# Kernel tuning notes

Hardware: AMD Instinct MI355X
Metric: run time of the kernel (lower is better)

The kernel has to match this reference:

```python
import jax, jax.numpy as jnp
import numpy as np

N = 50000        # nodes
E = 1600000      # edges
R = 20           # relations (num_rels, num_bases == num_rels -> per-relation weights)
IN = 4           # in_dim
H = 64           # hidden_dim
L = 4            # total RGCN layers (num_hidden_layers=3 hidden + 1 output)
EPS = 1e-5       # BatchNorm eps


def setup_inputs() -> dict:
    key = jax.random.key(0)
    ks = jax.random.split(key, 14)
    x = jax.random.normal(ks[0], (N, IN), jnp.float32)
    edge_index = jax.random.randint(ks[1], (2, E), 0, N, jnp.int32)
    edge_type = jax.random.randint(ks[2], (E,), 0, R, jnp.int32)
    # RGCN layer 0: in_dim -> hidden
    W0 = jax.random.normal(ks[3], (R, IN, H), jnp.float32) * 0.1
    root0 = jax.random.normal(ks[4], (IN, H), jnp.float32) * 0.1
    b0 = jax.random.normal(ks[5], (H,), jnp.float32) * 0.1
    # RGCN layers 1..3: hidden -> hidden (stacked)
    Wh = jax.random.normal(ks[6], (L - 1, R, H, H), jnp.float32) * 0.1
    rooth = jax.random.normal(ks[7], (L - 1, H, H), jnp.float32) * 0.1
    bh = jax.random.normal(ks[8], (L - 1, H), jnp.float32) * 0.1
    # BatchNorm (eval mode: running stats) per layer
    gamma = 1.0 + 0.1 * jax.random.normal(ks[9], (L, H), jnp.float32)
    beta = 0.1 * jax.random.normal(ks[10], (L, H), jnp.float32)
    run_mean = 0.1 * jax.random.normal(ks[11], (L, H), jnp.float32)
    run_var = jax.random.uniform(ks[12], (L, H), jnp.float32, 0.5, 1.5)
    return {"x": x, "edge_index": edge_index, "edge_type": edge_type,
            "W0": W0, "root0": root0, "b0": b0,
            "Wh": Wh, "rooth": rooth, "bh": bh,
            "gamma": gamma, "beta": beta,
            "run_mean": run_mean, "run_var": run_var}


def _rgcn(h, src, dst, seg, inv_cnt, W, root, bias):
    # mean-aggregate source features per (relation, dst) segment, then per-relation GEMM
    msum = jax.ops.segment_sum(h[src], seg, num_segments=R * N)  # [R*N, F]
    agg = (msum * inv_cnt).reshape(R, N, -1)                     # [R, N, F]
    return jnp.einsum('rni,rio->no', agg, W) + h @ root + bias   # [N, out]


def _bn_eval(h, g, b, rm, rv):
    return (h - rm) * (g * jax.lax.rsqrt(rv + EPS)) + b


def reference(x, edge_index, edge_type, W0, root0, b0, Wh, rooth, bh,
              gamma, beta, run_mean, run_var):
    src, dst = edge_index[0], edge_index[1]
    seg = edge_type * N + dst  # [E], segment id per (relation, dst)
    cnt = jax.ops.segment_sum(jnp.ones((E,), x.dtype), seg, num_segments=R * N)
    inv_cnt = (1.0 / jnp.maximum(cnt, 1.0))[:, None]  # mean aggregation per relation
    h = x
    for i in range(L):
        W, root, b = (W0, root0, b0) if i == 0 else (Wh[i - 1], rooth[i - 1], bh[i - 1])
        h = _rgcn(h, src, dst, seg, inv_cnt, W, root, b)
        h = _bn_eval(h, gamma[i], beta[i], run_mean[i], run_var[i])
    # last layer (i == num_hidden_layers): relu (dropout is identity in eval)
    return jax.nn.relu(h)
```

## Files before the change

### kernel.cpp

```cpp
#include <hip/hip_runtime.h>

#define NN 50000
#define NE 1600000
#define RR 20
#define BN_EPS 1e-5f
#define SCAN_NB ((NN + 1023) / 1024)

typedef __attribute__((ext_vector_type(8))) short bf16x8;
typedef __attribute__((ext_vector_type(4))) float f32x4;

__device__ __forceinline__ unsigned short f2bf(float f) {
    unsigned u = __float_as_uint(f);
    u += 0x7fff + ((u >> 16) & 1);
    return (unsigned short)(u >> 16);
}
__device__ __forceinline__ void unpack8(uint4 r, float* v) {
    v[0] = __uint_as_float(r.x << 16); v[1] = __uint_as_float(r.x & 0xffff0000u);
    v[2] = __uint_as_float(r.y << 16); v[3] = __uint_as_float(r.y & 0xffff0000u);
    v[4] = __uint_as_float(r.z << 16); v[5] = __uint_as_float(r.z & 0xffff0000u);
    v[6] = __uint_as_float(r.w << 16); v[7] = __uint_as_float(r.w & 0xffff0000u);
}

__global__ void count_kernel(const int* __restrict__ dst, const int* __restrict__ et,
                             int* __restrict__ cnt) {
    int stride = gridDim.x * blockDim.x;
    for (int e = blockIdx.x * blockDim.x + threadIdx.x; e < NE; e += stride)
        atomicAdd(&cnt[dst[e] * RR + et[e]], 1);
}

__global__ void deg_kernel(const int* __restrict__ cnt, int* __restrict__ deg) {
    int stride = gridDim.x * blockDim.x;
    for (int n = blockIdx.x * blockDim.x + threadIdx.x; n < NN; n += stride) {
        int s = 0;
        #pragma unroll
        for (int r = 0; r < RR; ++r) s += cnt[n * RR + r];
        deg[n] = s;
    }
}

__global__ __launch_bounds__(256) void scan1_kernel(const int* __restrict__ in,
                                                    int* __restrict__ out,
                                                    int* __restrict__ bsums, int n) {
    __shared__ int lds[256];
    int tid  = threadIdx.x;
    int base = blockIdx.x * 1024 + tid * 4;
    int v[4];
    #pragma unroll
    for (int j = 0; j < 4; ++j) v[j] = (base + j < n) ? in[base + j] : 0;
    int tsum = v[0] + v[1] + v[2] + v[3];
    lds[tid] = tsum;
    __syncthreads();
    for (int off = 1; off < 256; off <<= 1) {
        int t = (tid >= off) ? lds[tid - off] : 0;
        __syncthreads();
        lds[tid] += t;
        __syncthreads();
    }
    int run = lds[tid] - tsum;
    #pragma unroll
    for (int j = 0; j < 4; ++j) {
        if (base + j < n) out[base + j] = run;
        run += v[j];
    }
    if (tid == 255) bsums[blockIdx.x] = lds[255];
}

__global__ __launch_bounds__(1024) void scan_top_kernel(int* __restrict__ bsums, int nb) {
    __shared__ int lds[1024];
    int tid = threadIdx.x;
    int v = (tid < nb) ? bsums[tid] : 0;
    lds[tid] = v;
    __syncthreads();
    for (int off = 1; off < 1024; off <<= 1) {
        int t = (tid >= off) ? lds[tid - off] : 0;
        __syncthreads();
        lds[tid] += t;
        __syncthreads();
    }
    bsums[tid] = lds[tid] - v;
}

__global__ void scan_add_kernel(int* __restrict__ out, const int* __restrict__ bsums, int n) {
    int stride = gridDim.x * blockDim.x;
    int i = blockIdx.x * blockDim.x + threadIdx.x;
    if (i == 0) out[NN] = NE;
    for (; i < n; i += stride)
        out[i] += bsums[i >> 10];
}

__global__ void fill_kernel(const int* __restrict__ src, const int* __restrict__ dst,
                            const int* __restrict__ et, const int* __restrict__ offs,
                            const int* __restrict__ cntdr,
                            int* __restrict__ fill, uint2* __restrict__ ep) {
    int stride = gridDim.x * blockDim.x;
    for (int e = blockIdx.x * blockDim.x + threadIdx.x; e < NE; e += stride) {
        int d = dst[e], r = et[e];
        int pos = offs[d] + atomicAdd(&fill[d], 1);
        int c = cntdr[d * RR + r];
        float ic = 1.0f / (float)(c > 0 ? c : 1);
        ep[pos] = make_uint2((unsigned)src[e] | ((unsigned)r << 20),
                             __float_as_uint(ic));
    }
}

__global__ __launch_bounds__(256) void wprep_kernel(const float* __restrict__ Wh,
                                                    const float* __restrict__ rooth,
                                                    unsigned short* __restrict__ Wt) {
    int l = blockIdx.x / 21, r = blockIdx.x % 21;
    const float* Ws = (r < 20) ? Wh + ((size_t)l * 20 + r) * 4096
                               : rooth + (size_t)l * 4096;
    unsigned short* Wd = Wt + ((size_t)l * 21 + r) * 4096;
    int t = threadIdx.x;
    int n4 = (t & 15) * 4;
    for (int k = t >> 4; k < 64; k += 16) {
        float4 w = *(const float4*)&Ws[(size_t)k * 64 + n4];
        Wd[(n4 + 0) * 64 + k] = f2bf(w.x);
        Wd[(n4 + 1) * 64 + k] = f2bf(w.y);
        Wd[(n4 + 2) * 64 + k] = f2bf(w.z);
        Wd[(n4 + 3) * 64 + k] = f2bf(w.w);
    }
}

__global__ __launch_bounds__(256) void xform0_kernel(
    const float* __restrict__ x, const float* __restrict__ W0,
    const float* __restrict__ root0, unsigned short* __restrict__ T,
    int c0, int nr) {
    __shared__ float Wl[21 * 256];
    int tid = threadIdx.x;
    for (int i = tid; i < 21 * 256; i += 256)
        Wl[i] = (i < 20 * 256) ? W0[i] : root0[i - 20 * 256];
    __syncthreads();
    int wslot = (blockIdx.x * 256 + tid) >> 6;
    int nw    = (gridDim.x * 256) >> 6;
    int col   = tid & 63;
    for (int n = wslot; n < NN; n += nw) {
        float4 xv = *(const float4*)&x[(size_t)n * 4];
        for (int r = 0; r < nr; ++r) {
            const float* w = &Wl[(c0 + r) * 256];
            float acc = xv.x * w[col] + xv.y * w[64 + col] +
                        xv.z * w[128 + col] + xv.w * w[192 + col];
            T[((size_t)r * NN + n) * 64 + col] = f2bf(acc);
        }
    }
}

__global__ __launch_bounds__(256) void xform_kernel(
    const unsigned short* __restrict__ hin, const unsigned short* __restrict__ WtL,
    unsigned short* __restrict__ T, int c0, int nr) {
    __shared__ unsigned short tile[64 * 72];
    const int tid  = threadIdx.x;
    const int n0   = blockIdx.x * 64;
    const int wv   = tid >> 6;
    const int lane = tid & 63;
    const int frow = lane & 15;
    const int kgrp = lane >> 4;
    int arc = min(n0 + wv * 16 + frow, NN - 1);
    bf16x8 a0 = *(const bf16x8*)&hin[(size_t)arc * 64 + kgrp * 8];
    bf16x8 a1 = *(const bf16x8*)&hin[(size_t)arc * 64 + 32 + kgrp * 8];
    for (int r = 0; r < nr; ++r) {
        const unsigned short* Wr = WtL + (size_t)(c0 + r) * 4096;
        unsigned short* Tr = T + (size_t)r * NN * 64;
        #pragma unroll
        for (int cf = 0; cf < 4; ++cf) {
            bf16x8 b0 = *(const bf16x8*)&Wr[(cf * 16 + frow) * 64 + kgrp * 8];
            bf16x8 b1 = *(const bf16x8*)&Wr[(cf * 16 + frow) * 64 + 32 + kgrp * 8];
            f32x4 d = {0.f, 0.f, 0.f, 0.f};
            d = __builtin_amdgcn_mfma_f32_16x16x32_bf16(a0, b0, d, 0, 0, 0);
            d = __builtin_amdgcn_mfma_f32_16x16x32_bf16(a1, b1, d, 0, 0, 0);
            #pragma unroll
            for (int j = 0; j < 4; ++j)
                tile[(wv * 16 + kgrp * 4 + j) * 72 + cf * 16 + frow] = f2bf(d[j]);
        }
        __syncthreads();
        #pragma unroll
        for (int i = tid; i < 512; i += 256) {
            int row = i >> 3, c16 = i & 7;
            int node = n0 + row;
            if (node < NN)
                *(uint4*)&Tr[(size_t)node * 64 + c16 * 8] =
                    *(const uint4*)&tile[row * 72 + c16 * 8];
        }
        __syncthreads();
    }
}

template <bool FIRST, bool LASTP, bool LASTL>
__global__ __launch_bounds__(256) void agg_kernel(
    const unsigned short* __restrict__ T, const int* __restrict__ offs,
    const uint2* __restrict__ ep, float* __restrict__ accum, int c0, int c1,
    const float* __restrict__ bias, const float* __restrict__ gamma,
    const float* __restrict__ beta, const float* __restrict__ rmean,
    const float* __restrict__ rvar, unsigned short* __restrict__ outb,
    float* __restrict__ outf) {
    constexpr bool FULL = FIRST && LASTP;
    int wid   = (blockIdx.x * 256 + threadIdx.x) >> 6;
    int nw    = (gridDim.x * 256) >> 6;
    int lane  = threadIdx.x & 63;
    int eslot = lane >> 3;
    int flane = lane & 7;
    const unsigned ce = (c1 < RR) ? (unsigned)c1 : (unsigned)RR;

    for (int n = wid; n < NN; n += nw) {
        int e0 = offs[n], e1 = offs[n + 1];
        float a[8] = {0, 0, 0, 0, 0, 0, 0, 0};
        for (int e = e0 + eslot; e < e1; e += 8) {
            uint2 m = ep[e];
            unsigned r = m.x >> 20;
            if (FULL || (r >= (unsigned)c0 && r < ce)) {
                float ic = __uint_as_float(m.y);
                size_t ti = ((size_t)(r - c0) * NN + (m.x & 0xFFFFF)) * 64;
                uint4 row = *(const uint4*)&T[ti + flane * 8];
                float v[8]; unpack8(row, v);
                #pragma unroll
                for (int j = 0; j < 8; ++j) a[j] += ic * v[j];
            }
        }
        #pragma unroll
        for (int off = 8; off < 64; off <<= 1)
            #pragma unroll
            for (int j = 0; j < 8; ++j) a[j] += __shfl_xor(a[j], off);

        if (eslot == 0) {
            if (LASTP) {
                uint4 rr = *(const uint4*)&T[((size_t)(20 - c0) * NN + n) * 64 + flane * 8];
                float rv[8]; unpack8(rr, rv);
                #pragma unroll
                for (int j = 0; j < 8; ++j) a[j] += rv[j];
            }
            if (!FIRST) {
                float4 p0 = *(const float4*)&accum[(size_t)n * 64 + flane * 8];
                float4 p1 = *(const float4*)&accum[(size_t)n * 64 + flane * 8 + 4];
                a[0] += p0.x; a[1] += p0.y; a[2] += p0.z; a[3] += p0.w;
                a[4] += p1.x; a[5] += p1.y; a[6] += p1.z; a[7] += p1.w;
            }
            if (!LASTP) {
                *(float4*)&accum[(size_t)n * 64 + flane * 8] =
                    make_float4(a[0], a[1], a[2], a[3]);
                *(float4*)&accum[(size_t)n * 64 + flane * 8 + 4] =
                    make_float4(a[4], a[5], a[6], a[7]);
            } else {
                float v[8];
                #pragma unroll
                for (int j = 0; j < 8; ++j) {
                    int col = flane * 8 + j;
                    float s = gamma[col] * rsqrtf(rvar[col] + BN_EPS);
                    v[j] = (a[j] + bias[col] - rmean[col]) * s + beta[col];
                }
                if (LASTL) {
                    float4 o0 = make_float4(fmaxf(v[0],0.f), fmaxf(v[1],0.f),
                                            fmaxf(v[2],0.f), fmaxf(v[3],0.f));
                    float4 o1 = make_float4(fmaxf(v[4],0.f), fmaxf(v[5],0.f),
                                            fmaxf(v[6],0.f), fmaxf(v[7],0.f));
                    *(float4*)&outf[(size_t)n * 64 + flane * 8]     = o0;
                    *(float4*)&outf[(size_t)n * 64 + flane * 8 + 4] = o1;
                } else {
                    ushort4 p0, p1;
                    p0.x = f2bf(v[0]); p0.y = f2bf(v[1]);
                    p0.z = f2bf(v[2]); p0.w = f2bf(v[3]);
                    p1.x = f2bf(v[4]); p1.y = f2bf(v[5]);
                    p1.z = f2bf(v[6]); p1.w = f2bf(v[7]);
                    *(ushort4*)&outb[(size_t)n * 64 + flane * 8]     = p0;
                    *(ushort4*)&outb[(size_t)n * 64 + flane * 8 + 4] = p1;
                }
            }
        }
    }
}

extern "C" void kernel_launch(void* const* d_in, const int* in_sizes, int n_in,
                              void* d_out, int out_size, void* d_ws, size_t ws_size,
                              hipStream_t stream) {
    const float* x     = (const float*)d_in[0];
    const int*   ei    = (const int*)d_in[1];
    const int*   et    = (const int*)d_in[2];
    const float* W0    = (const float*)d_in[3];
    const float* root0 = (const float*)d_in[4];
    const float* b0    = (const float*)d_in[5];
    const float* Wh    = (const float*)d_in[6];
    const float* rooth = (const float*)d_in[7];
    const float* bh    = (const float*)d_in[8];
    const float* gamma = (const float*)d_in[9];
    const float* beta  = (const float*)d_in[10];
    const float* rmean = (const float*)d_in[11];
    const float* rvar  = (const float*)d_in[12];
    float* out = (float*)d_out;

    const int* src = ei;
    const int* dst = ei + NE;

    int*   cntdr = (int*)d_ws;
    int*   deg   = cntdr + 1000000;
    int*   fill  = deg + 50000;
    int*   offs  = fill + 50000;
    int*   bsums = offs + 50004;
    uint2* ep    = (uint2*)(bsums + 1024);
    unsigned short* Wt = (unsigned short*)(ep + NE);
    unsigned short* h0 = Wt + 3 * 21 * 4096;
    unsigned short* h1 = h0 + NN * 64;
    float* accum = (float*)(h1 + NN * 64);
    unsigned short* T = (unsigned short*)(accum + NN * 64);

    size_t used  = (size_t)((char*)T - (char*)d_ws);
    size_t avail = (ws_size > used) ? ws_size - used : 0;
    size_t per   = (size_t)NN * 64 * 2;
    int nrel = (int)(avail / per);
    if (nrel < 1) nrel = 1;
    if (nrel > 21) nrel = 21;
    int npass = (21 + nrel - 1) / nrel;

    hipMemsetAsync(cntdr, 0, (size_t)NN * RR * sizeof(int), stream);
    hipMemsetAsync(fill, 0, (size_t)NN * sizeof(int), stream);
    count_kernel<<<2048, 256, 0, stream>>>(dst, et, cntdr);
    deg_kernel<<<256, 256, 0, stream>>>(cntdr, deg);
    scan1_kernel<<<SCAN_NB, 256, 0, stream>>>(deg, offs, bsums, NN);
    scan_top_kernel<<<1, 1024, 0, stream>>>(bsums, SCAN_NB);
    scan_add_kernel<<<256, 256, 0, stream>>>(offs, bsums, NN);
    fill_kernel<<<2048, 256, 0, stream>>>(src, dst, et, offs, cntdr, fill, ep);
    wprep_kernel<<<63, 256, 0, stream>>>(Wh, rooth, Wt);

    const int XB = (NN + 63) / 64;

    for (int l = 0; l < 4; ++l) {
        const unsigned short* hin = (l == 2) ? h1 : h0;
        unsigned short* hout = (l == 1) ? h1 : h0;
        const float* bl  = (l == 0) ? b0 : bh + (size_t)(l - 1) * 64;
        const float* gl  = gamma + (size_t)l * 64;
        const float* btl = beta + (size_t)l * 64;
        const float* rml = rmean + (size_t)l * 64;
        const float* rvl = rvar + (size_t)l * 64;
        int c0 = 0;
        for (int p = 0; p < npass; ++p) {
            int c1 = c0 + nrel; if (c1 > 21) c1 = 21;
            if (l == 0)
                xform0_kernel<<<2048, 256, 0, stream>>>(x, W0, root0, T, c0, c1 - c0);
            else
                xform_kernel<<<XB, 256, 0, stream>>>(
                    hin, Wt + (size_t)(l - 1) * 21 * 4096, T, c0, c1 - c0);
            bool first = (p == 0), lastp = (p == npass - 1);
            bool lastl = lastp && (l == 3);
            #define AGG(F, LP, LL) agg_kernel<F, LP, LL><<<2048, 256, 0, stream>>>( \
                T, offs, ep, accum, c0, c1, bl, gl, btl, rml, rvl, hout, out)
            if (first && lastp && lastl)      AGG(true,  true,  true);
            else if (first && lastp)          AGG(true,  true,  false);
            else if (first)                   AGG(true,  false, false);
            else if (lastp && lastl)          AGG(false, true,  true);
            else if (lastp)                   AGG(false, true,  false);
            else                              AGG(false, false, false);
            #undef AGG
            c0 = c1;
        }
    }
}
```

Baseline: 791.3 us.

## Fuse layer-0 transform into edge aggregation and parallelize xform over relations

Layer 0 now uses a dedicated aggregation kernel that reads the 4-wide input features per edge and applies the per-relation 4x64 weight from shared memory on the fly, then adds the root term, bias and BatchNorm. This removes the materialisation of 21 transformed relation tables for layer 0 and the separate xform0 pass. The hidden-layer xform kernel also spreads relations across a second grid dimension instead of looping over them inside one block, which raises parallelism. The cost is more per-edge arithmetic in layer 0 and a re-read of the A fragment for each relation block.

```diff
diff --git a/kernel.cpp b/kernel.cpp
--- a/kernel.cpp
+++ b/kernel.cpp
@@ -121,35 +121,78 @@
     }
 }
 
-__global__ __launch_bounds__(256) void xform0_kernel(
-    const float* __restrict__ x, const float* __restrict__ W0,
-    const float* __restrict__ root0, unsigned short* __restrict__ T,
-    int c0, int nr) {
+__global__ __launch_bounds__(256) void agg0_kernel(
+    const float* __restrict__ x, const int* __restrict__ offs,
+    const uint2* __restrict__ ep,
+    const float* __restrict__ W0, const float* __restrict__ root0,
+    const float* __restrict__ b0, const float* __restrict__ gamma,
+    const float* __restrict__ beta, const float* __restrict__ rmean,
+    const float* __restrict__ rvar, unsigned short* __restrict__ outb) {
     __shared__ float Wl[21 * 256];
     int tid = threadIdx.x;
     for (int i = tid; i < 21 * 256; i += 256)
         Wl[i] = (i < 20 * 256) ? W0[i] : root0[i - 20 * 256];
     __syncthreads();
-    int wslot = (blockIdx.x * 256 + tid) >> 6;
+
+    int wid   = (blockIdx.x * 256 + tid) >> 6;
     int nw    = (gridDim.x * 256) >> 6;
-    int col   = tid & 63;
-    for (int n = wslot; n < NN; n += nw) {
-        float4 xv = *(const float4*)&x[(size_t)n * 4];
-        for (int r = 0; r < nr; ++r) {
-            const float* w = &Wl[(c0 + r) * 256];
-            float acc = xv.x * w[col] + xv.y * w[64 + col] +
-                        xv.z * w[128 + col] + xv.w * w[192 + col];
-            T[((size_t)r * NN + n) * 64 + col] = f2bf(acc);
+    int lane  = tid & 63;
+    int eslot = lane >> 3;
+    int flane = lane & 7;
+
+    for (int n = wid; n < NN; n += nw) {
+        int e0 = offs[n], e1 = offs[n + 1];
+        float a[8] = {0, 0, 0, 0, 0, 0, 0, 0};
+        for (int e = e0 + eslot; e < e1; e += 8) {
+            uint2 m = ep[e];
+            float ic = __uint_as_float(m.y);
+            float4 xv = *(const float4*)&x[(size_t)(m.x & 0xFFFFF) * 4];
+            const float* w = &Wl[(m.x >> 20) * 256 + flane * 8];
+            float4 w0 = *(const float4*)&w[0],   w0b = *(const float4*)&w[4];
+            float4 w1 = *(const float4*)&w[64],  w1b = *(const float4*)&w[68];
+            float4 w2 = *(const float4*)&w[128], w2b = *(const float4*)&w[132];
+            float4 w3 = *(const float4*)&w[192], w3b = *(const float4*)&w[196];
+            a[0] += ic * (xv.x * w0.x + xv.y * w1.x + xv.z * w2.x + xv.w * w3.x);
+            a[1] += ic * (xv.x * w0.y + xv.y * w1.y + xv.z * w2.y + xv.w * w3.y);
+            a[2] += ic * (xv.x * w0.z + xv.y * w1.z + xv.z * w2.z + xv.w * w3.z);
+            a[3] += ic * (xv.x * w0.w + xv.y * w1.w + xv.z * w2.w + xv.w * w3.w);
+            a[4] += ic * (xv.x * w0b.x + xv.y * w1b.x + xv.z * w2b.x + xv.w * w3b.x);
+            a[5] += ic * (xv.x * w0b.y + xv.y * w1b.y + xv.z * w2b.y + xv.w * w3b.y);
+            a[6] += ic * (xv.x * w0b.z + xv.y * w1b.z + xv.z * w2b.z + xv.w * w3b.z);
+            a[7] += ic * (xv.x * w0b.w + xv.y * w1b.w + xv.z * w2b.w + xv.w * w3b.w);
+        }
+        #pragma unroll
+        for (int off = 8; off < 64; off <<= 1)
+            #pragma unroll
+            for (int j = 0; j < 8; ++j) a[j] += __shfl_xor(a[j], off);
+
+        if (eslot == 0) {
+            float4 xn = *(const float4*)&x[(size_t)n * 4];
+            const float* w = &Wl[20 * 256 + flane * 8];
+            float v[8];
+            #pragma unroll
+            for (int j = 0; j < 8; ++j) {
+                a[j] += xn.x * w[j] + xn.y * w[64 + j] + xn.z * w[128 + j] + xn.w * w[192 + j];
+                int col = flane * 8 + j;
+                float s = gamma[col] * rsqrtf(rvar[col] + BN_EPS);
+                v[j] = (a[j] + b0[col] - rmean[col]) * s + beta[col];
+            }
+            ushort4 p0, p1;
+            p0.x = f2bf(v[0]); p0.y = f2bf(v[1]); p0.z = f2bf(v[2]); p0.w = f2bf(v[3]);
+            p1.x = f2bf(v[4]); p1.y = f2bf(v[5]); p1.z = f2bf(v[6]); p1.w = f2bf(v[7]);
+            *(ushort4*)&outb[(size_t)n * 64 + flane * 8]     = p0;
+            *(ushort4*)&outb[(size_t)n * 64 + flane * 8 + 4] = p1;
         }
     }
 }
 
 __global__ __launch_bounds__(256) void xform_kernel(
     const unsigned short* __restrict__ hin, const unsigned short* __restrict__ WtL,
-    unsigned short* __restrict__ T, int c0, int nr) {
+    unsigned short* __restrict__ T, int c0) {
     __shared__ unsigned short tile[64 * 72];
     const int tid  = threadIdx.x;
     const int n0   = blockIdx.x * 64;
+    const int r    = blockIdx.y;
     const int wv   = tid >> 6;
     const int lane = tid & 63;
     const int frow = lane & 15;
@@ -157,30 +200,27 @@
     int arc = min(n0 + wv * 16 + frow, NN - 1);
     bf16x8 a0 = *(const bf16x8*)&hin[(size_t)arc * 64 + kgrp * 8];
     bf16x8 a1 = *(const bf16x8*)&hin[(size_t)arc * 64 + 32 + kgrp * 8];
-    for (int r = 0; r < nr; ++r) {
-        const unsigned short* Wr = WtL + (size_t)(c0 + r) * 4096;
-        unsigned short* Tr = T + (size_t)r * NN * 64;
+    const unsigned short* Wr = WtL + (size_t)(c0 + r) * 4096;
+    unsigned short* Tr = T + (size_t)r * NN * 64;
+    #pragma unroll
+    for (int cf = 0; cf < 4; ++cf) {
+        bf16x8 b0 = *(const bf16x8*)&Wr[(cf * 16 + frow) * 64 + kgrp * 8];
+        bf16x8 b1 = *(const bf16x8*)&Wr[(cf * 16 + frow) * 64 + 32 + kgrp * 8];
+        f32x4 d = {0.f, 0.f, 0.f, 0.f};
+        d = __builtin_amdgcn_mfma_f32_16x16x32_bf16(a0, b0, d, 0, 0, 0);
+        d = __builtin_amdgcn_mfma_f32_16x16x32_bf16(a1, b1, d, 0, 0, 0);
         #pragma unroll
-        for (int cf = 0; cf < 4; ++cf) {
-            bf16x8 b0 = *(const bf16x8*)&Wr[(cf * 16 + frow) * 64 + kgrp * 8];
-            bf16x8 b1 = *(const bf16x8*)&Wr[(cf * 16 + frow) * 64 + 32 + kgrp * 8];
-            f32x4 d = {0.f, 0.f, 0.f, 0.f};
-            d = __builtin_amdgcn_mfma_f32_16x16x32_bf16(a0, b0, d, 0, 0, 0);
-            d = __builtin_amdgcn_mfma_f32_16x16x32_bf16(a1, b1, d, 0, 0, 0);
-            #pragma unroll
-            for (int j = 0; j < 4; ++j)
-                tile[(wv * 16 + kgrp * 4 + j) * 72 + cf * 16 + frow] = f2bf(d[j]);
-        }
-        __syncthreads();
-        #pragma unroll
-        for (int i = tid; i < 512; i += 256) {
-            int row = i >> 3, c16 = i & 7;
-            int node = n0 + row;
-            if (node < NN)
-                *(uint4*)&Tr[(size_t)node * 64 + c16 * 8] =
-                    *(const uint4*)&tile[row * 72 + c16 * 8];
-        }
-        __syncthreads();
+        for (int j = 0; j < 4; ++j)
+            tile[(wv * 16 + kgrp * 4 + j) * 72 + cf * 16 + frow] = f2bf(d[j]);
+    }
+    __syncthreads();
+    #pragma unroll
+    for (int i = tid; i < 512; i += 256) {
+        int row = i >> 3, c16 = i & 7;
+        int node = n0 + row;
+        if (node < NN)
+            *(uint4*)&Tr[(size_t)node * 64 + c16 * 8] =
+                *(const uint4*)&tile[row * 72 + c16 * 8];
     }
 }
 
@@ -318,12 +358,14 @@
     fill_kernel<<<2048, 256, 0, stream>>>(src, dst, et, offs, cntdr, fill, ep);
     wprep_kernel<<<63, 256, 0, stream>>>(Wh, rooth, Wt);
 
+    agg0_kernel<<<2048, 256, 0, stream>>>(
+        x, offs, ep, W0, root0, b0, gamma, beta, rmean, rvar, h0);
+
     const int XB = (NN + 63) / 64;
-
-    for (int l = 0; l < 4; ++l) {
+    for (int l = 1; l < 4; ++l) {
         const unsigned short* hin = (l == 2) ? h1 : h0;
         unsigned short* hout = (l == 1) ? h1 : h0;
-        const float* bl  = (l == 0) ? b0 : bh + (size_t)(l - 1) * 64;
+        const float* bl  = bh + (size_t)(l - 1) * 64;
         const float* gl  = gamma + (size_t)l * 64;
         const float* btl = beta + (size_t)l * 64;
         const float* rml = rmean + (size_t)l * 64;
@@ -331,11 +373,9 @@
         int c0 = 0;
         for (int p = 0; p < npass; ++p) {
             int c1 = c0 + nrel; if (c1 > 21) c1 = 21;
-            if (l == 0)
-                xform0_kernel<<<2048, 256, 0, stream>>>(x, W0, root0, T, c0, c1 - c0);
-            else
-                xform_kernel<<<XB, 256, 0, stream>>>(
-                    hin, Wt + (size_t)(l - 1) * 21 * 4096, T, c0, c1 - c0);
+            dim3 xg(XB, c1 - c0);
+            xform_kernel<<<xg, 256, 0, stream>>>(
+                hin, Wt + (size_t)(l - 1) * 21 * 4096, T, c0);
             bool first = (p == 0), lastp = (p == npass - 1);
             bool lastl = lastp && (l == 3);
             #define AGG(F, LP, LL) agg_kernel<F, LP, LL><<<2048, 256, 0, stream>>>( \
```

New measurement: 734.5 us. 1.08x faster.
